# Kernel optimization log

Hardware: AMD Instinct MI355X
Metric: run time of the kernel (lower is better)

## Reference

```python
import jax, jax.numpy as jnp
import numpy as np

D_MODEL = 768
NUM_HEADS = 12
D_K = D_MODEL // NUM_HEADS


def setup_inputs() -> dict:
    key = jax.random.key(0)
    ks = jax.random.split(key, 11)
    B, S = 2, 2048
    sc = 1.0 / np.sqrt(D_MODEL)
    return {
        "q": jax.random.normal(ks[0], (B, S, D_MODEL), jnp.float32),
        "k": jax.random.normal(ks[1], (B, S, D_MODEL), jnp.float32),
        "v": jax.random.normal(ks[2], (B, S, D_MODEL), jnp.float32),
        "w_q": jax.random.normal(ks[3], (D_MODEL, D_MODEL), jnp.float32) * sc,
        "b_q": jnp.zeros((D_MODEL,), jnp.float32),
        "w_k": jax.random.normal(ks[4], (D_MODEL, D_MODEL), jnp.float32) * sc,
        "b_k": jnp.zeros((D_MODEL,), jnp.float32),
        "w_v": jax.random.normal(ks[5], (D_MODEL, D_MODEL), jnp.float32) * sc,
        "b_v": jnp.zeros((D_MODEL,), jnp.float32),
        "w_o": jax.random.normal(ks[6], (D_MODEL, D_MODEL), jnp.float32) * sc,
        "b_o": jnp.zeros((D_MODEL,), jnp.float32),
    }


def _split_heads(x, B):
    # [B, S, D] -> [B, H, S, d_k]
    return x.reshape(B, -1, NUM_HEADS, D_K).transpose(0, 2, 1, 3)


def reference(q, k, v, w_q, b_q, w_k, b_k, w_v, b_v, w_o, b_o):
    B = q.shape[0]
    # torch nn.Linear: y = x @ W.T + b; weights stored [out, in]
    qh = _split_heads(q @ w_q.T + b_q, B)
    kh = _split_heads(k @ w_k.T + b_k, B)
    vh = _split_heads(v @ w_v.T + b_v, B)
    scores = jnp.einsum("bhsd,bhtd->bhst", qh, kh) / jnp.sqrt(jnp.float32(D_K))
    attn = jax.nn.softmax(scores, axis=-1)
    ctx = jnp.einsum("bhst,bhtd->bhsd", attn, vh)
    ctx = ctx.transpose(0, 2, 1, 3).reshape(B, -1, D_MODEL)
    return ctx @ w_o.T + b_o
```

## Files before the change

kernel.cpp:

```cpp
#include <hip/hip_runtime.h>
#include <cstdint>


#define S_LEN 2048
#define NHEAD 12
#define DMODEL 768

typedef short s16x8 __attribute__((ext_vector_type(8)));
typedef float f32x4 __attribute__((ext_vector_type(4)));
typedef float f32x16 __attribute__((ext_vector_type(16)));

#define MFMA16(a, b, c) __builtin_amdgcn_mfma_f32_16x16x32_bf16((a), (b), (c), 0, 0, 0)
#define MFMA32(a, b, c) __builtin_amdgcn_mfma_f32_32x32x16_bf16((a), (b), (c), 0, 0, 0)

__device__ __forceinline__ void lds_dma16(void* lds, const void* g) {
  __builtin_amdgcn_global_load_lds(
      (const __attribute__((address_space(1))) unsigned int*)g,
      (__attribute__((address_space(3))) unsigned int*)lds, 16, 0, 0);
}

__device__ __forceinline__ unsigned int pk_bf16(float a, float b) {
  unsigned int ua = __float_as_uint(a), ub = __float_as_uint(b);
  ua = (ua + 0x7FFFu + ((ua >> 16) & 1u)) >> 16;
  ub = (ub + 0x7FFFu + ((ub >> 16) & 1u)) >> 16;
  return ua | (ub << 16);
}
__device__ __forceinline__ short bf16r(float a) {
  unsigned int ua = __float_as_uint(a);
  return (short)((ua + 0x7FFFu + ((ua >> 16) & 1u)) >> 16);
}
__device__ __forceinline__ unsigned int pk_trunc(float a, float b) {
  return __builtin_amdgcn_perm(__float_as_uint(b), __float_as_uint(a), 0x07060302u);
}
__device__ __forceinline__ float bf16_floor(float a) {
  return __uint_as_float(__float_as_uint(a) & 0xFFFF0000u);
}

__global__ __launch_bounds__(256)
void convert_all(const float* __restrict__ q, const float* __restrict__ k,
                 const float* __restrict__ v,
                 const float* __restrict__ w0, const float* __restrict__ w1,
                 const float* __restrict__ w2, const float* __restrict__ w3,
                 short* __restrict__ qb, short* __restrict__ kb,
                 short* __restrict__ vb,
                 short* __restrict__ o0, short* __restrict__ o1,
                 short* __restrict__ o2, short* __restrict__ o3) {
  int b = blockIdx.x;
  const float* src;
  short* dst;
  if (b < 9216) {
    const int s = b / 3072;
    src = (s == 0) ? q : (s == 1) ? k : v;
    dst = (s == 0) ? qb : (s == 1) ? kb : vb;
    b -= s * 3072;
  } else {
    b -= 9216;
    const int s = b / 576;
    src = (s == 0) ? w0 : (s == 1) ? w1 : (s == 2) ? w2 : w3;
    dst = (s == 0) ? o0 : (s == 1) ? o1 : (s == 2) ? o2 : o3;
    b -= s * 576;
  }
  const long i = ((long)b * 256 + threadIdx.x) * 4;
  float4 f = *(const float4*)(src + i);
  uint2 u;
  u.x = pk_bf16(f.x, f.y);
  u.y = pk_bf16(f.z, f.w);
  *(uint2*)(dst + i) = u;
}

__global__ __launch_bounds__(256)
void qkv_kernel(const short* __restrict__ qb, const short* __restrict__ kb,
                const short* __restrict__ vb,
                const short* __restrict__ wq, const short* __restrict__ wk,
                const short* __restrict__ wv,
                const float* __restrict__ bq, const float* __restrict__ bk,
                const float* __restrict__ bv,
                short* __restrict__ qh, short* __restrict__ kh,
                short* __restrict__ vt) {
  constexpr int K = 768;
  __shared__ short Abuf[128 * 64];
  __shared__ short Bbuf[128 * 64];

  const int L   = blockIdx.x;
  const int xcd = L & 7;
  const int i   = L >> 3;
  const int nt  = i % 6;
  const int pl  = xcd * 12 + i / 6;
  const int z   = pl >> 5;
  const int mt  = pl & 31;
  const int m0  = mt * 128;
  const int n0  = nt * 128;

  const short* A = (z == 0) ? qb : (z == 1) ? kb : vb;
  const short* B = (z == 0) ? wq : (z == 1) ? wk : wv;
  const float* bias = (z == 0) ? bq : (z == 1) ? bk : bv;

  const int tid  = threadIdx.x;
  const int lane = tid & 63;
  const int w    = tid >> 6;
  const int g    = lane >> 4;
  const int c    = lane & 15;
  const int wm   = (w & 1) * 64;
  const int wn   = (w >> 1) * 64;

  const int lr   = lane >> 3;
  const int dchk = ((lane & 7) ^ lr) * 8;
  const short* Ag = A + (long)(m0 + w * 32 + lr) * K + dchk;
  const short* Bg = B + (long)(n0 + w * 32 + lr) * K + dchk;
  short* Al = &Abuf[(w * 32) * 64];
  short* Bl = &Bbuf[(w * 32) * 64];

  f32x4 acc[4][4];
#pragma unroll
  for (int a = 0; a < 4; ++a)
#pragma unroll
    for (int b2 = 0; b2 < 4; ++b2) acc[a][b2] = (f32x4){0.f, 0.f, 0.f, 0.f};

  int aoff[4][2], boff[4][2];
#pragma unroll
  for (int mb = 0; mb < 4; ++mb)
#pragma unroll
    for (int kk = 0; kk < 2; ++kk) {
      const int Ra = wm + mb * 16 + c;
      const int Rb = wn + mb * 16 + c;
      aoff[mb][kk] = Ra * 64 + (((kk * 4 + g) ^ (Ra & 7)) * 8);
      boff[mb][kk] = Rb * 64 + (((kk * 4 + g) ^ (Rb & 7)) * 8);
    }

  for (int kt = 0; kt < K; kt += 64) {
#pragma unroll
    for (int ii = 0; ii < 4; ++ii) {
      lds_dma16(Al + ii * 8 * 64, Ag + (long)ii * 8 * K + kt);
      lds_dma16(Bl + ii * 8 * 64, Bg + (long)ii * 8 * K + kt);
    }
    __syncthreads();

#pragma unroll
    for (int kk = 0; kk < 2; ++kk) {
      s16x8 af[4], bf[4];
#pragma unroll
      for (int mb = 0; mb < 4; ++mb)
        af[mb] = *(const s16x8*)&Abuf[aoff[mb][kk]];
#pragma unroll
      for (int nb = 0; nb < 4; ++nb)
        bf[nb] = *(const s16x8*)&Bbuf[boff[nb][kk]];
#pragma unroll
      for (int mb = 0; mb < 4; ++mb)
#pragma unroll
        for (int nb = 0; nb < 4; ++nb)
          acc[mb][nb] = MFMA16(af[mb], bf[nb], acc[mb][nb]);
    }
    __syncthreads();
  }

  if (z < 2) {
    short* outp = z ? kh : qh;
    const float scale = z ? 1.0f : 0.18033688011112042f;
#pragma unroll
    for (int mb = 0; mb < 4; ++mb) {
#pragma unroll
      for (int nb = 0; nb < 4; ++nb) {
        const int n = n0 + wn + nb * 16 + c;
        const float bvv = bias[n];
        const int hh = n >> 6, d = n & 63;
#pragma unroll
        for (int r = 0; r < 4; ++r) {
          const int m = m0 + wm + mb * 16 + g * 4 + r;
          const int b2 = m >> 11, s = m & 2047;
          const float val = (acc[mb][nb][r] + bvv) * scale;
          outp[(((long)(b2 * NHEAD + hh) * S_LEN + s) << 6) + d] = bf16r(val);
        }
      }
    }
  } else {
#pragma unroll
    for (int mb = 0; mb < 4; ++mb) {
#pragma unroll
      for (int nb = 0; nb < 4; ++nb) {
        const int n = n0 + wn + nb * 16 + c;
        const float bvv = bias[n];
        const int hh = n >> 6, d = n & 63;
        const int m_base = m0 + wm + mb * 16 + g * 4;
        const int b2 = m_base >> 11, t = m_base & 2047;
        uint2 ov;
        ov.x = pk_bf16(acc[mb][nb][0] + bvv, acc[mb][nb][1] + bvv);
        ov.y = pk_bf16(acc[mb][nb][2] + bvv, acc[mb][nb][3] + bvv);
        *(uint2*)(vt + ((long)(b2 * NHEAD + hh) * 64 + d) * S_LEN + t) = ov;
      }
    }
  }
}

__global__ __launch_bounds__(256)
void o_kernel(const short* __restrict__ ctx, const short* __restrict__ wo,
              const float* __restrict__ bo, float* __restrict__ out) {
  constexpr int K = 768;
  __shared__ short Abuf[64 * 64];
  __shared__ short Bbuf[128 * 64];

  const int L   = blockIdx.x;
  const int xcd = L & 7;
  const int i   = L >> 3;
  const int nt  = i % 6;
  const int mt  = xcd * 8 + i / 6;
  const int m0  = mt * 64;
  const int n0  = nt * 128;

  const int tid  = threadIdx.x;
  const int lane = tid & 63;
  const int w    = tid >> 6;
  const int g    = lane >> 4;
  const int c    = lane & 15;
  const int wm   = (w & 1) * 32;
  const int wn   = (w >> 1) * 64;

  const int lr   = lane >> 3;
  const int dchk = ((lane & 7) ^ lr) * 8;
  const short* Ag = ctx + (long)(m0 + w * 16 + lr) * K + dchk;
  const short* Bg = wo + (long)(n0 + w * 32 + lr) * K + dchk;
  short* Al = &Abuf[(w * 16) * 64];
  short* Bl = &Bbuf[(w * 32) * 64];

  f32x4 acc[2][4];
#pragma unroll
  for (int a = 0; a < 2; ++a)
#pragma unroll
    for (int b2 = 0; b2 < 4; ++b2) acc[a][b2] = (f32x4){0.f, 0.f, 0.f, 0.f};

  int aoff[2][2], boff[4][2];
#pragma unroll
  for (int kk = 0; kk < 2; ++kk) {
#pragma unroll
    for (int mb = 0; mb < 2; ++mb) {
      const int Ra = wm + mb * 16 + c;
      aoff[mb][kk] = Ra * 64 + (((kk * 4 + g) ^ (Ra & 7)) * 8);
    }
#pragma unroll
    for (int nb = 0; nb < 4; ++nb) {
      const int Rb = wn + nb * 16 + c;
      boff[nb][kk] = Rb * 64 + (((kk * 4 + g) ^ (Rb & 7)) * 8);
    }
  }

  for (int kt = 0; kt < K; kt += 64) {
#pragma unroll
    for (int ii = 0; ii < 2; ++ii)
      lds_dma16(Al + ii * 8 * 64, Ag + (long)ii * 8 * K + kt);
#pragma unroll
    for (int ii = 0; ii < 4; ++ii)
      lds_dma16(Bl + ii * 8 * 64, Bg + (long)ii * 8 * K + kt);
    __syncthreads();

#pragma unroll
    for (int kk = 0; kk < 2; ++kk) {
      s16x8 af[2], bf[4];
#pragma unroll
      for (int mb = 0; mb < 2; ++mb)
        af[mb] = *(const s16x8*)&Abuf[aoff[mb][kk]];
#pragma unroll
      for (int nb = 0; nb < 4; ++nb)
        bf[nb] = *(const s16x8*)&Bbuf[boff[nb][kk]];
#pragma unroll
      for (int mb = 0; mb < 2; ++mb)
#pragma unroll
        for (int nb = 0; nb < 4; ++nb)
          acc[mb][nb] = MFMA16(af[mb], bf[nb], acc[mb][nb]);
    }
    __syncthreads();
  }

#pragma unroll
  for (int mb = 0; mb < 2; ++mb) {
#pragma unroll
    for (int nb = 0; nb < 4; ++nb) {
      const int n = n0 + wn + nb * 16 + c;
      const float bvv = bo[n];
#pragma unroll
      for (int r = 0; r < 4; ++r) {
        const int m = m0 + wm + mb * 16 + g * 4 + r;
        out[(long)m * DMODEL + n] = acc[mb][nb][r] + bvv;
      }
    }
  }
}

__global__ __launch_bounds__(256, 3)
void attn_kernel(const short* __restrict__ Qh, const short* __restrict__ Kh,
                 const short* __restrict__ Vt, short* __restrict__ Ctx) {
  __shared__ short kbuf[2][64 * 64];
  __shared__ short vbuf[2][64 * 64];

  const int tid  = threadIdx.x;
  const int lane = tid & 63;
  const int w    = tid >> 6;
  const int par  = w & 1;
  const int rh   = w >> 1;
  const int q32  = lane & 31;
  const int hi   = lane >> 5;
  const int bh   = blockIdx.y;
  const int qs0  = blockIdx.x * 64;
  const long base = (long)bh * S_LEN * 64;
  const short* Qb = Qh + base;
  const short* Kb = Kh + base;
  const short* Vb = Vt + base;

  const long qrow = (long)(qs0 + rh * 32 + q32) * 64;
  s16x8 qf[4];
#pragma unroll
  for (int db = 0; db < 4; ++db)
    qf[db] = *(const s16x8*)(Qb + qrow + db * 16 + hi * 8);

  f32x16 co0, co1;
#pragma unroll
  for (int i = 0; i < 16; ++i) { co0[i] = 0.f; co1[i] = 0.f; }
  float l_lane = 0.f;

  const int srow = tid >> 2;
  const int sq   = tid & 3;
  const int sw   = srow & 7;
  const int sg0  = ((2 * sq)     ^ sw) * 8;
  const int sg1  = ((2 * sq + 1) ^ sw) * 8;
  const short* kg = Kb + (long)srow * 64 + sq * 16;
  const short* vg = Vb + (long)srow * S_LEN + sq * 16;

  uint4 rkE0, rkE1, rvE0, rvE1, rkO0, rkO1, rvO0, rvO1;
  auto fetch_pair = [&](long tE, long tO) {
    rkE0 = *(const uint4*)(kg + tE * 64);
    rkE1 = *(const uint4*)(kg + tE * 64 + 8);
    rvE0 = *(const uint4*)(vg + tE);
    rvE1 = *(const uint4*)(vg + tE + 8);
    rkO0 = *(const uint4*)(kg + tO * 64);
    rkO1 = *(const uint4*)(kg + tO * 64 + 8);
    rvO0 = *(const uint4*)(vg + tO);
    rvO1 = *(const uint4*)(vg + tO + 8);
  };
  auto store_pair = [&]() {
    *(uint4*)&kbuf[0][srow * 64 + sg0] = rkE0;
    *(uint4*)&kbuf[0][srow * 64 + sg1] = rkE1;
    *(uint4*)&vbuf[0][srow * 64 + sg0] = rvE0;
    *(uint4*)&vbuf[0][srow * 64 + sg1] = rvE1;
    *(uint4*)&kbuf[1][srow * 64 + sg0] = rkO0;
    *(uint4*)&kbuf[1][srow * 64 + sg1] = rkO1;
    *(uint4*)&vbuf[1][srow * 64 + sg0] = rvO0;
    *(uint4*)&vbuf[1][srow * 64 + sg1] = rvO1;
  };

  const int tw = lane & 7;
  int c4[4];
#pragma unroll
  for (int i = 0; i < 4; ++i) c4[i] = ((2 * i + hi) ^ tw) * 8;
  const int row0 = q32 * 64;
  const int row1 = (32 + q32) * 64;
  const short* kb2 = kbuf[par];
  const short* vb2 = vbuf[par];

  auto mkfrag = [&](unsigned a, unsigned b, unsigned c, unsigned d) -> s16x8 {
    asm("v_permlane32_swap_b32 %0, %1" : "+v"(a), "+v"(c));
    asm("v_permlane32_swap_b32 %0, %1" : "+v"(b), "+v"(d));
    uint4 u;
    u.x = a; u.y = b; u.z = c; u.w = d;
    return __builtin_bit_cast(s16x8, u);
  };

  auto step = [&]() {
    f32x16 s0, s1;
#pragma unroll
    for (int i = 0; i < 16; ++i) { s0[i] = 0.f; s1[i] = 0.f; }
    __builtin_amdgcn_s_setprio(1);
#pragma unroll
    for (int db = 0; db < 4; ++db) {
      const s16x8 k0 = *(const s16x8*)&kb2[row0 + c4[db]];
      const s16x8 k1 = *(const s16x8*)&kb2[row1 + c4[db]];
      s0 = MFMA32(k0, qf[db], s0);
      s1 = MFMA32(k1, qf[db], s1);
    }
    __builtin_amdgcn_s_setprio(0);
    unsigned pk0[8], pk1[8];
    float la = 0.f, lb = 0.f;
#pragma unroll
    for (int i = 0; i < 8; ++i) {
      float a0 = __builtin_amdgcn_exp2f(s0[2 * i]);
      float b0 = __builtin_amdgcn_exp2f(s0[2 * i + 1]);
      float a1 = __builtin_amdgcn_exp2f(s1[2 * i]);
      float b1 = __builtin_amdgcn_exp2f(s1[2 * i + 1]);
      la += bf16_floor(a0) + bf16_floor(b0);
      lb += bf16_floor(a1) + bf16_floor(b1);
      pk0[i] = pk_trunc(a0, b0);
      pk1[i] = pk_trunc(a1, b1);
    }
    l_lane += la + lb;
    s16x8 pf0 = mkfrag(pk0[0], pk0[1], pk0[2], pk0[3]);
    s16x8 pf1 = mkfrag(pk0[4], pk0[5], pk0[6], pk0[7]);
    s16x8 pf2 = mkfrag(pk1[0], pk1[1], pk1[2], pk1[3]);
    s16x8 pf3 = mkfrag(pk1[4], pk1[5], pk1[6], pk1[7]);
    __builtin_amdgcn_s_setprio(1);
#pragma unroll
    for (int sl = 0; sl < 4; ++sl) {
      const s16x8 v0 = *(const s16x8*)&vb2[row0 + c4[sl]];
      const s16x8 v1 = *(const s16x8*)&vb2[row1 + c4[sl]];
      const s16x8 pf = (sl == 0) ? pf0 : (sl == 1) ? pf1 : (sl == 2) ? pf2 : pf3;
      co0 = MFMA32(v0, pf, co0);
      co1 = MFMA32(v1, pf, co1);
    }
    __builtin_amdgcn_s_setprio(0);
  };

  constexpr int NT = S_LEN / 64;
  fetch_pair(0, 64);
  store_pair();
  for (int ph = 0; ph < NT / 2; ++ph) {
    __syncthreads();
    const long tE = (2 * ph + 2 < NT) ? (long)(2 * ph + 2) * 64 : 0;
    const long tO = (2 * ph + 3 < NT) ? (long)(2 * ph + 3) * 64 : 0;
    fetch_pair(tE, tO);
    step();
    __syncthreads();
    store_pair();
  }

  float rs = l_lane + __shfl_xor(l_lane, 32);

  __syncthreads();
  float* mbuf = (float*)((rh == 0) ? (short*)kbuf : (short*)vbuf);
  float* mp = mbuf + lane * 36;
  if (par) {
#pragma unroll
    for (int i = 0; i < 4; ++i) {
      *(float4*)(mp + 4 * i)      = make_float4(co0[4*i], co0[4*i+1], co0[4*i+2], co0[4*i+3]);
      *(float4*)(mp + 16 + 4 * i) = make_float4(co1[4*i], co1[4*i+1], co1[4*i+2], co1[4*i+3]);
    }
    mp[32] = rs;
  }
  __syncthreads();
  if (!par) {
#pragma unroll
    for (int i = 0; i < 4; ++i) {
      float4 a = *(const float4*)(mp + 4 * i);
      float4 b = *(const float4*)(mp + 16 + 4 * i);
      co0[4*i] += a.x; co0[4*i+1] += a.y; co0[4*i+2] += a.z; co0[4*i+3] += a.w;
      co1[4*i] += b.x; co1[4*i+1] += b.y; co1[4*i+2] += b.z; co1[4*i+3] += b.w;
    }
    rs += mp[32];
    const float invl = 1.f / rs;

    const int hh = bh % NHEAD;
    const long tok = (long)(bh / NHEAD) * S_LEN + qs0 + rh * 32 + q32;
    short* outp = Ctx + tok * DMODEL + hh * 64;
#pragma unroll
    for (int rq = 0; rq < 4; ++rq) {
      const int d0 = 8 * rq + 4 * hi;
      uint2 ov;
      ov.x = pk_bf16(co0[4*rq] * invl, co0[4*rq+1] * invl);
      ov.y = pk_bf16(co0[4*rq+2] * invl, co0[4*rq+3] * invl);
      *(uint2*)(outp + d0) = ov;
      uint2 ov2;
      ov2.x = pk_bf16(co1[4*rq] * invl, co1[4*rq+1] * invl);
      ov2.y = pk_bf16(co1[4*rq+2] * invl, co1[4*rq+3] * invl);
      *(uint2*)(outp + 32 + d0) = ov2;
    }
  }
}

extern "C" void kernel_launch(void* const* d_in, const int* in_sizes, int n_in,
                              void* d_out, int out_size, void* d_ws, size_t ws_size,
                              hipStream_t stream) {
  const float* q   = (const float*)d_in[0];
  const float* k   = (const float*)d_in[1];
  const float* v   = (const float*)d_in[2];
  const float* w_q = (const float*)d_in[3];
  const float* b_q = (const float*)d_in[4];
  const float* w_k = (const float*)d_in[5];
  const float* b_k = (const float*)d_in[6];
  const float* w_v = (const float*)d_in[7];
  const float* b_v = (const float*)d_in[8];
  const float* w_o = (const float*)d_in[9];
  const float* b_o = (const float*)d_in[10];
  float* out = (float*)d_out;

  const long NELEM = (long)2 * NHEAD * S_LEN * 64;
  const long WELEM = (long)DMODEL * DMODEL;
  short* qh  = (short*)d_ws;
  short* kh  = qh + NELEM;
  short* vt  = kh + NELEM;
  short* wqb = vt + NELEM;
  short* wkb = wqb + WELEM;
  short* wvb = wkb + WELEM;
  short* wob = wvb + WELEM;
  short* qb  = wob + WELEM;
  short* kb  = qb + NELEM;
  short* vb  = kb + NELEM;
  short* ctx = qb;

  dim3 blk(256);
  convert_all<<<dim3(11520), blk, 0, stream>>>(q, k, v, w_q, w_k, w_v, w_o,
                                               qb, kb, vb, wqb, wkb, wvb, wob);
  qkv_kernel<<<dim3(576), blk, 0, stream>>>(qb, kb, vb, wqb, wkb, wvb,
                                            b_q, b_k, b_v, qh, kh, vt);
  attn_kernel<<<dim3(32, 24), blk, 0, stream>>>(qh, kh, vt, ctx);
  o_kernel<<<dim3(384), blk, 0, stream>>>(ctx, wob, b_o, out);
}
```

Measured before the change: 187.8 us.

## Double-buffer LDS tiles in QKV and output projection GEMMs

```diff
diff --git a/kernel.cpp b/kernel.cpp
--- a/kernel.cpp
+++ b/kernel.cpp
@@ -78,8 +78,8 @@
                 short* __restrict__ qh, short* __restrict__ kh,
                 short* __restrict__ vt) {
   constexpr int K = 768;
-  __shared__ short Abuf[128 * 64];
-  __shared__ short Bbuf[128 * 64];
+  __shared__ short Ab[2][128 * 64];
+  __shared__ short Bb[2][128 * 64];
 
   const int L   = blockIdx.x;
   const int xcd = L & 7;
@@ -107,8 +107,16 @@
   const int dchk = ((lane & 7) ^ lr) * 8;
   const short* Ag = A + (long)(m0 + w * 32 + lr) * K + dchk;
   const short* Bg = B + (long)(n0 + w * 32 + lr) * K + dchk;
-  short* Al = &Abuf[(w * 32) * 64];
-  short* Bl = &Bbuf[(w * 32) * 64];
+
+  auto stage = [&](int p, int kt) {
+    short* Al = &Ab[p][(w * 32) * 64];
+    short* Bl = &Bb[p][(w * 32) * 64];
+#pragma unroll
+    for (int ii = 0; ii < 4; ++ii) {
+      lds_dma16(Al + ii * 8 * 64, Ag + (long)ii * 8 * K + kt);
+      lds_dma16(Bl + ii * 8 * 64, Bg + (long)ii * 8 * K + kt);
+    }
+  };
 
   f32x4 acc[4][4];
 #pragma unroll
@@ -127,23 +135,22 @@
       boff[mb][kk] = Rb * 64 + (((kk * 4 + g) ^ (Rb & 7)) * 8);
     }
 
-  for (int kt = 0; kt < K; kt += 64) {
-#pragma unroll
-    for (int ii = 0; ii < 4; ++ii) {
-      lds_dma16(Al + ii * 8 * 64, Ag + (long)ii * 8 * K + kt);
-      lds_dma16(Bl + ii * 8 * 64, Bg + (long)ii * 8 * K + kt);
-    }
-    __syncthreads();
-
+  stage(0, 0);
+  __syncthreads();
+  int cur = 0;
+  for (int it = 0; it < 12; ++it) {
+    if (it < 11) stage(cur ^ 1, (it + 1) * 64);
+    const short* Ac = Ab[cur];
+    const short* Bc = Bb[cur];
 #pragma unroll
     for (int kk = 0; kk < 2; ++kk) {
       s16x8 af[4], bf[4];
 #pragma unroll
       for (int mb = 0; mb < 4; ++mb)
-        af[mb] = *(const s16x8*)&Abuf[aoff[mb][kk]];
+        af[mb] = *(const s16x8*)&Ac[aoff[mb][kk]];
 #pragma unroll
       for (int nb = 0; nb < 4; ++nb)
-        bf[nb] = *(const s16x8*)&Bbuf[boff[nb][kk]];
+        bf[nb] = *(const s16x8*)&Bc[boff[nb][kk]];
 #pragma unroll
       for (int mb = 0; mb < 4; ++mb)
 #pragma unroll
@@ -151,6 +158,7 @@
           acc[mb][nb] = MFMA16(af[mb], bf[nb], acc[mb][nb]);
     }
     __syncthreads();
+    cur ^= 1;
   }
 
   if (z < 2) {
@@ -195,8 +203,8 @@
 void o_kernel(const short* __restrict__ ctx, const short* __restrict__ wo,
               const float* __restrict__ bo, float* __restrict__ out) {
   constexpr int K = 768;
-  __shared__ short Abuf[64 * 64];
-  __shared__ short Bbuf[128 * 64];
+  __shared__ short Ab[2][64 * 64];
+  __shared__ short Bb[2][128 * 64];
 
   const int L   = blockIdx.x;
   const int xcd = L & 7;
@@ -218,8 +226,17 @@
   const int dchk = ((lane & 7) ^ lr) * 8;
   const short* Ag = ctx + (long)(m0 + w * 16 + lr) * K + dchk;
   const short* Bg = wo + (long)(n0 + w * 32 + lr) * K + dchk;
-  short* Al = &Abuf[(w * 16) * 64];
-  short* Bl = &Bbuf[(w * 32) * 64];
+
+  auto stage = [&](int p, int kt) {
+    short* Al = &Ab[p][(w * 16) * 64];
+    short* Bl = &Bb[p][(w * 32) * 64];
+#pragma unroll
+    for (int ii = 0; ii < 2; ++ii)
+      lds_dma16(Al + ii * 8 * 64, Ag + (long)ii * 8 * K + kt);
+#pragma unroll
+    for (int ii = 0; ii < 4; ++ii)
+      lds_dma16(Bl + ii * 8 * 64, Bg + (long)ii * 8 * K + kt);
+  };
 
   f32x4 acc[2][4];
 #pragma unroll
@@ -242,24 +259,22 @@
     }
   }
 
-  for (int kt = 0; kt < K; kt += 64) {
-#pragma unroll
-    for (int ii = 0; ii < 2; ++ii)
-      lds_dma16(Al + ii * 8 * 64, Ag + (long)ii * 8 * K + kt);
-#pragma unroll
-    for (int ii = 0; ii < 4; ++ii)
-      lds_dma16(Bl + ii * 8 * 64, Bg + (long)ii * 8 * K + kt);
-    __syncthreads();
-
+  stage(0, 0);
+  __syncthreads();
+  int cur = 0;
+  for (int it = 0; it < 12; ++it) {
+    if (it < 11) stage(cur ^ 1, (it + 1) * 64);
+    const short* Ac = Ab[cur];
+    const short* Bc = Bb[cur];
 #pragma unroll
     for (int kk = 0; kk < 2; ++kk) {
       s16x8 af[2], bf[4];
 #pragma unroll
       for (int mb = 0; mb < 2; ++mb)
-        af[mb] = *(const s16x8*)&Abuf[aoff[mb][kk]];
+        af[mb] = *(const s16x8*)&Ac[aoff[mb][kk]];
 #pragma unroll
       for (int nb = 0; nb < 4; ++nb)
-        bf[nb] = *(const s16x8*)&Bbuf[boff[nb][kk]];
+        bf[nb] = *(const s16x8*)&Bc[boff[nb][kk]];
 #pragma unroll
       for (int mb = 0; mb < 2; ++mb)
 #pragma unroll
@@ -267,6 +282,7 @@
           acc[mb][nb] = MFMA16(af[mb], bf[nb], acc[mb][nb]);
     }
     __syncthreads();
+    cur ^= 1;
   }
 
 #pragma unroll
```

New measurement: 190.8 us. About the same (+1.6%).

## Split attention work by key half per wave to reuse K fragments

Applied to the files above, without the earlier changes.

```diff
diff --git a/kernel.cpp b/kernel.cpp
--- a/kernel.cpp
+++ b/kernel.cpp
@@ -284,7 +284,7 @@
   }
 }
 
-__global__ __launch_bounds__(256, 3)
+__global__ __launch_bounds__(256, 2)
 void attn_kernel(const short* __restrict__ Qh, const short* __restrict__ Kh,
                  const short* __restrict__ Vt, short* __restrict__ Ctx) {
   __shared__ short kbuf[2][64 * 64];
@@ -294,7 +294,7 @@
   const int lane = tid & 63;
   const int w    = tid >> 6;
   const int par  = w & 1;
-  const int rh   = w >> 1;
+  const int th   = w >> 1;
   const int q32  = lane & 31;
   const int hi   = lane >> 5;
   const int bh   = blockIdx.y;
@@ -304,16 +304,23 @@
   const short* Kb = Kh + base;
   const short* Vb = Vt + base;
 
-  const long qrow = (long)(qs0 + rh * 32 + q32) * 64;
-  s16x8 qf[4];
-#pragma unroll
-  for (int db = 0; db < 4; ++db)
-    qf[db] = *(const s16x8*)(Qb + qrow + db * 16 + hi * 8);
-
-  f32x16 co0, co1;
-#pragma unroll
-  for (int i = 0; i < 16; ++i) { co0[i] = 0.f; co1[i] = 0.f; }
-  float l_lane = 0.f;
+  s16x8 qfA[4], qfB[4];
+  {
+    const long qrA = (long)(qs0 + q32) * 64;
+    const long qrB = (long)(qs0 + 32 + q32) * 64;
+#pragma unroll
+    for (int db = 0; db < 4; ++db) {
+      qfA[db] = *(const s16x8*)(Qb + qrA + db * 16 + hi * 8);
+      qfB[db] = *(const s16x8*)(Qb + qrB + db * 16 + hi * 8);
+    }
+  }
+
+  f32x16 coA0, coA1, coB0, coB1;
+#pragma unroll
+  for (int i = 0; i < 16; ++i) {
+    coA0[i] = 0.f; coA1[i] = 0.f; coB0[i] = 0.f; coB1[i] = 0.f;
+  }
+  float lA = 0.f, lB = 0.f;
 
   const int srow = tid >> 2;
   const int sq   = tid & 3;
@@ -349,8 +356,12 @@
   int c4[4];
 #pragma unroll
   for (int i = 0; i < 4; ++i) c4[i] = ((2 * i + hi) ^ tw) * 8;
+  int ct[2];
+#pragma unroll
+  for (int sl = 0; sl < 2; ++sl) ct[sl] = ((4 * th + 2 * sl + hi) ^ tw) * 8;
   const int row0 = q32 * 64;
   const int row1 = (32 + q32) * 64;
+  const int rowK = th ? row1 : row0;
   const short* kb2 = kbuf[par];
   const short* vb2 = vbuf[par];
 
@@ -363,44 +374,48 @@
   };
 
   auto step = [&]() {
-    f32x16 s0, s1;
-#pragma unroll
-    for (int i = 0; i < 16; ++i) { s0[i] = 0.f; s1[i] = 0.f; }
+    s16x8 kf[4];
+#pragma unroll
+    for (int db = 0; db < 4; ++db)
+      kf[db] = *(const s16x8*)&kb2[rowK + c4[db]];
+    f32x16 sA, sB;
+#pragma unroll
+    for (int i = 0; i < 16; ++i) { sA[i] = 0.f; sB[i] = 0.f; }
     __builtin_amdgcn_s_setprio(1);
 #pragma unroll
-    for (int db = 0; db < 4; ++db) {
-      const s16x8 k0 = *(const s16x8*)&kb2[row0 + c4[db]];
-      const s16x8 k1 = *(const s16x8*)&kb2[row1 + c4[db]];
-      s0 = MFMA32(k0, qf[db], s0);
-      s1 = MFMA32(k1, qf[db], s1);
-    }
+    for (int db = 0; db < 4; ++db) sA = MFMA32(kf[db], qfA[db], sA);
+#pragma unroll
+    for (int db = 0; db < 4; ++db) sB = MFMA32(kf[db], qfB[db], sB);
     __builtin_amdgcn_s_setprio(0);
-    unsigned pk0[8], pk1[8];
+    unsigned pkA[8], pkB[8];
     float la = 0.f, lb = 0.f;
 #pragma unroll
     for (int i = 0; i < 8; ++i) {
-      float a0 = __builtin_amdgcn_exp2f(s0[2 * i]);
-      float b0 = __builtin_amdgcn_exp2f(s0[2 * i + 1]);
-      float a1 = __builtin_amdgcn_exp2f(s1[2 * i]);
-      float b1 = __builtin_amdgcn_exp2f(s1[2 * i + 1]);
-      la += bf16_floor(a0) + bf16_floor(b0);
-      lb += bf16_floor(a1) + bf16_floor(b1);
-      pk0[i] = pk_trunc(a0, b0);
-      pk1[i] = pk_trunc(a1, b1);
-    }
-    l_lane += la + lb;
-    s16x8 pf0 = mkfrag(pk0[0], pk0[1], pk0[2], pk0[3]);
-    s16x8 pf1 = mkfrag(pk0[4], pk0[5], pk0[6], pk0[7]);
-    s16x8 pf2 = mkfrag(pk1[0], pk1[1], pk1[2], pk1[3]);
-    s16x8 pf3 = mkfrag(pk1[4], pk1[5], pk1[6], pk1[7]);
+      float a0 = __builtin_amdgcn_exp2f(sA[2 * i]);
+      float a1 = __builtin_amdgcn_exp2f(sA[2 * i + 1]);
+      la += bf16_floor(a0) + bf16_floor(a1);
+      pkA[i] = pk_trunc(a0, a1);
+      float b0 = __builtin_amdgcn_exp2f(sB[2 * i]);
+      float b1 = __builtin_amdgcn_exp2f(sB[2 * i + 1]);
+      lb += bf16_floor(b0) + bf16_floor(b1);
+      pkB[i] = pk_trunc(b0, b1);
+    }
+    lA += la;
+    lB += lb;
+    s16x8 pfA[2], pfB[2];
+    pfA[0] = mkfrag(pkA[0], pkA[1], pkA[2], pkA[3]);
+    pfA[1] = mkfrag(pkA[4], pkA[5], pkA[6], pkA[7]);
+    pfB[0] = mkfrag(pkB[0], pkB[1], pkB[2], pkB[3]);
+    pfB[1] = mkfrag(pkB[4], pkB[5], pkB[6], pkB[7]);
     __builtin_amdgcn_s_setprio(1);
 #pragma unroll
-    for (int sl = 0; sl < 4; ++sl) {
-      const s16x8 v0 = *(const s16x8*)&vb2[row0 + c4[sl]];
-      const s16x8 v1 = *(const s16x8*)&vb2[row1 + c4[sl]];
-      const s16x8 pf = (sl == 0) ? pf0 : (sl == 1) ? pf1 : (sl == 2) ? pf2 : pf3;
-      co0 = MFMA32(v0, pf, co0);
-      co1 = MFMA32(v1, pf, co1);
+    for (int sl = 0; sl < 2; ++sl) {
+      const s16x8 v0 = *(const s16x8*)&vb2[row0 + ct[sl]];
+      const s16x8 v1 = *(const s16x8*)&vb2[row1 + ct[sl]];
+      coA0 = MFMA32(v0, pfA[sl], coA0);
+      coA1 = MFMA32(v1, pfA[sl], coA1);
+      coB0 = MFMA32(v0, pfB[sl], coB0);
+      coB1 = MFMA32(v1, pfB[sl], coB1);
     }
     __builtin_amdgcn_s_setprio(0);
   };
@@ -418,45 +433,72 @@
     store_pair();
   }
 
-  float rs = l_lane + __shfl_xor(l_lane, 32);
-
-  __syncthreads();
-  float* mbuf = (float*)((rh == 0) ? (short*)kbuf : (short*)vbuf);
-  float* mp = mbuf + lane * 36;
-  if (par) {
+  float rsA = lA + __shfl_xor(lA, 32);
+  float rsB = lB + __shfl_xor(lB, 32);
+
+  float* RK = (float*)kbuf;
+  float* RV = (float*)vbuf;
+  auto dump = [&](float* R, const f32x16& x0, const f32x16& x1, float rs) {
+    float* mp = R + lane * 36;
 #pragma unroll
     for (int i = 0; i < 4; ++i) {
-      *(float4*)(mp + 4 * i)      = make_float4(co0[4*i], co0[4*i+1], co0[4*i+2], co0[4*i+3]);
-      *(float4*)(mp + 16 + 4 * i) = make_float4(co1[4*i], co1[4*i+1], co1[4*i+2], co1[4*i+3]);
+      *(float4*)(mp + 4 * i)      = make_float4(x0[4*i], x0[4*i+1], x0[4*i+2], x0[4*i+3]);
+      *(float4*)(mp + 16 + 4 * i) = make_float4(x1[4*i], x1[4*i+1], x1[4*i+2], x1[4*i+3]);
     }
     mp[32] = rs;
-  }
-  __syncthreads();
-  if (!par) {
+  };
+  auto addin = [&](const float* R, f32x16& x0, f32x16& x1, float& rs) {
+    const float* mp = R + lane * 36;
 #pragma unroll
     for (int i = 0; i < 4; ++i) {
       float4 a = *(const float4*)(mp + 4 * i);
       float4 b = *(const float4*)(mp + 16 + 4 * i);
-      co0[4*i] += a.x; co0[4*i+1] += a.y; co0[4*i+2] += a.z; co0[4*i+3] += a.w;
-      co1[4*i] += b.x; co1[4*i+1] += b.y; co1[4*i+2] += b.z; co1[4*i+3] += b.w;
+      x0[4*i] += a.x; x0[4*i+1] += a.y; x0[4*i+2] += a.z; x0[4*i+3] += a.w;
+      x1[4*i] += b.x; x1[4*i+1] += b.y; x1[4*i+2] += b.z; x1[4*i+3] += b.w;
     }
     rs += mp[32];
-    const float invl = 1.f / rs;
+  };
+
+  __syncthreads();
+  if (par == 1) dump(th ? RV : RK, coA0, coA1, rsA);
+  __syncthreads();
+  if (par == 0) addin(th ? RV : RK, coA0, coA1, rsA);
+  __syncthreads();
+  if (par == 1) dump(th ? RV : RK, coB0, coB1, rsB);
+  __syncthreads();
+  if (par == 0) addin(th ? RV : RK, coB0, coB1, rsB);
+  __syncthreads();
+  if (par == 0 && th == 1) {
+    dump(RK, coA0, coA1, rsA);
+    dump(RV, coB0, coB1, rsB);
+  }
+  __syncthreads();
+  if (w == 0) {
+    addin(RK, coA0, coA1, rsA);
+    addin(RV, coB0, coB1, rsB);
+    const float invA = 1.f / rsA;
+    const float invB = 1.f / rsB;
 
     const int hh = bh % NHEAD;
-    const long tok = (long)(bh / NHEAD) * S_LEN + qs0 + rh * 32 + q32;
-    short* outp = Ctx + tok * DMODEL + hh * 64;
+    const long tokA = (long)(bh / NHEAD) * S_LEN + qs0 + q32;
+    short* opA = Ctx + tokA * DMODEL + hh * 64;
+    short* opB = opA + (long)32 * DMODEL;
 #pragma unroll
     for (int rq = 0; rq < 4; ++rq) {
       const int d0 = 8 * rq + 4 * hi;
       uint2 ov;
-      ov.x = pk_bf16(co0[4*rq] * invl, co0[4*rq+1] * invl);
-      ov.y = pk_bf16(co0[4*rq+2] * invl, co0[4*rq+3] * invl);
-      *(uint2*)(outp + d0) = ov;
-      uint2 ov2;
-      ov2.x = pk_bf16(co1[4*rq] * invl, co1[4*rq+1] * invl);
-      ov2.y = pk_bf16(co1[4*rq+2] * invl, co1[4*rq+3] * invl);
-      *(uint2*)(outp + 32 + d0) = ov2;
+      ov.x = pk_bf16(coA0[4*rq] * invA, coA0[4*rq+1] * invA);
+      ov.y = pk_bf16(coA0[4*rq+2] * invA, coA0[4*rq+3] * invA);
+      *(uint2*)(opA + d0) = ov;
+      ov.x = pk_bf16(coA1[4*rq] * invA, coA1[4*rq+1] * invA);
+      ov.y = pk_bf16(coA1[4*rq+2] * invA, coA1[4*rq+3] * invA);
+      *(uint2*)(opA + 32 + d0) = ov;
+      ov.x = pk_bf16(coB0[4*rq] * invB, coB0[4*rq+1] * invB);
+      ov.y = pk_bf16(coB0[4*rq+2] * invB, coB0[4*rq+3] * invB);
+      *(uint2*)(opB + d0) = ov;
+      ov.x = pk_bf16(coB1[4*rq] * invB, coB1[4*rq+1] * invB);
+      ov.y = pk_bf16(coB1[4*rq+2] * invB, coB1[4*rq+3] * invB);
+      *(uint2*)(opB + 32 + d0) = ov;
     }
   }
 }
```

After: 191.9 us. 2.2% more time.
